# Performance work log

Measured on AMD Instinct MI355X. Metric: run time of the kernel, lower is better.

Reference implementation:

```python
import jax, jax.numpy as jnp
import numpy as np

B, S, H, L = 64, 512, 768, 21


def setup_inputs() -> dict:
    key = jax.random.key(0)
    ks = jax.random.split(key, 8)
    hidden = jax.random.normal(ks[0], (B, S, H), dtype=jnp.float32)
    attention_mask = jnp.ones((B, S), dtype=jnp.int32)
    labels = jax.random.randint(ks[1], (B, S), 0, L, dtype=jnp.int64)
    W = jax.random.normal(ks[2], (H, L), dtype=jnp.float32) * 0.02
    b = jnp.zeros((L,), dtype=jnp.float32)
    start_transitions = jax.random.uniform(ks[3], (L,), minval=-0.1, maxval=0.1)
    end_transitions = jax.random.uniform(ks[4], (L,), minval=-0.1, maxval=0.1)
    transitions = jax.random.uniform(ks[5], (L, L), minval=-0.1, maxval=0.1)
    return {"hidden": hidden, "attention_mask": attention_mask, "labels": labels,
            "W": W, "b": b, "start_transitions": start_transitions,
            "end_transitions": end_transitions, "transitions": transitions}


def _crf_llh(emissions, tags, mask, start, end, trans):
    # torchcrf log-likelihood, batch_first. emissions [B,S,L], tags [B,S], mask [B,S] bool
    maskf = mask.astype(emissions.dtype)
    first_tags = tags[:, 0]
    num = start[first_tags] + jnp.take_along_axis(emissions[:, 0], first_tags[:, None], axis=1)[:, 0]
    trans_scores = trans[tags[:, :-1], tags[:, 1:]]                         # [B,S-1]
    emit_scores = jnp.take_along_axis(emissions, tags[:, :, None], axis=2)[:, :, 0]  # [B,S]
    num = num + jnp.sum((trans_scores + emit_scores[:, 1:]) * maskf[:, 1:], axis=1)
    seq_ends = jnp.sum(mask.astype(jnp.int32), axis=1) - 1
    last_tags = jnp.take_along_axis(tags, seq_ends[:, None], axis=1)[:, 0]
    num = num + end[last_tags]
    # denominator: forward algorithm as a scan over time
    def step(score, xs):
        emit_t, m_t = xs  # [B,L], [B]
        nxt = jax.nn.logsumexp(score[:, :, None] + trans[None] + emit_t[:, None, :], axis=1)
        return jnp.where(m_t[:, None], nxt, score), None
    score0 = start[None] + emissions[:, 0]
    xs = (jnp.transpose(emissions[:, 1:], (1, 0, 2)), mask[:, 1:].T)
    scoreT, _ = jax.lax.scan(step, score0, xs)
    denom = jax.nn.logsumexp(scoreT + end[None], axis=1)
    return num - denom


def _viterbi_one_hot(emissions, mask, start, end, trans):
    # Viterbi decode (max-plus scan) + backtrack, returns one-hot logits like _decoded_to_one_hot
    def fstep(score, xs):
        emit_t, m_t = xs
        cand = score[:, :, None] + trans[None]     # [B,L,L]
        idx = jnp.argmax(cand, axis=1)             # [B,L] best previous tag
        nxt = jnp.max(cand, axis=1) + emit_t
        return jnp.where(m_t[:, None], nxt, score), idx
    score0 = start[None] + emissions[:, 0]
    xs = (jnp.transpose(emissions[:, 1:], (1, 0, 2)), mask[:, 1:].T)
    scoreT, hist = jax.lax.scan(fstep, score0, xs)   # hist [S-1,B,L]
    best_last = jnp.argmax(scoreT + end[None], axis=1)  # [B]
    def bstep(carry, xs):
        h_t, m_t = xs
        prev = jnp.take_along_axis(h_t, carry[:, None], axis=1)[:, 0]
        return jnp.where(m_t, prev, carry), carry
    tag0, tags_rest = jax.lax.scan(bstep, best_last, (hist, mask[:, 1:].T), reverse=True)
    tags = jnp.concatenate([tag0[:, None], tags_rest.T], axis=1)  # [B,S]
    one_hot = jax.nn.one_hot(tags, emissions.shape[-1], dtype=emissions.dtype)
    return one_hot * mask[:, :, None].astype(emissions.dtype)


def reference(hidden, attention_mask, labels, W, b, start_transitions, end_transitions, transitions):
    mask = attention_mask.astype(bool)
    emissions = jnp.einsum('bsh,hl->bsl', hidden, W) + b  # classifier (dropout = identity in eval)
    logits = _viterbi_one_hot(emissions, mask, start_transitions, end_transitions, transitions)
    # loss path: replicate forward's tag/mask fixups
    tags = jnp.where(labels < 0, 0, labels).at[:, 0].set(0)
    valid = (mask & (labels >= 0)).at[:, 0].set(True)
    llh = _crf_llh(emissions, tags, valid, start_transitions, end_transitions, transitions)
    loss = -jnp.mean(llh)
    return loss, logits
```

## Files before the change

kernel.cpp:

```cpp
#include <hip/hip_runtime.h>
#include <math.h>

#define BB 64
#define SS 512
#define HH 768
#define LL 21
#define STR 513
#define INFF __builtin_huge_valf()

__device__ inline float rlf(float v, int i) {
    return __int_as_float(__builtin_amdgcn_readlane(__float_as_int(v), i));
}
__device__ inline float mx3(float a, float b, float c) { return fmaxf(fmaxf(a, b), c); }
__device__ inline float wmax64(float v) {
    #pragma unroll
    for (int off = 32; off; off >>= 1) v = fmaxf(v, __shfl_xor(v, off));
    return v;
}
__device__ inline float rlmax21(float a) {
    float r0 = mx3(rlf(a, 0), rlf(a, 1), rlf(a, 2));
    float r1 = mx3(rlf(a, 3), rlf(a, 4), rlf(a, 5));
    float r2 = mx3(rlf(a, 6), rlf(a, 7), rlf(a, 8));
    float r3 = mx3(rlf(a, 9), rlf(a, 10), rlf(a, 11));
    float r4 = mx3(rlf(a, 12), rlf(a, 13), rlf(a, 14));
    float r5 = mx3(rlf(a, 15), rlf(a, 16), rlf(a, 17));
    float r6 = mx3(rlf(a, 18), rlf(a, 19), rlf(a, 20));
    return mx3(mx3(r0, r1, r2), mx3(r3, r4, r5), r6);
}

__global__ __launch_bounds__(128) void k_emis(const float* __restrict__ hidden,
                                              const float* __restrict__ W,
                                              const float* __restrict__ bias,
                                              float* __restrict__ em0,
                                              float* __restrict__ em1,
                                              float* __restrict__ em2,
                                              float* __restrict__ em3) {
    __shared__ float Wl[192 * 24];
    int tid = threadIdx.x;
    int q = blockIdx.x & 3;
    int rg = blockIdx.x >> 2;
    int row = rg * 128 + tid;
    const float* hp = hidden + (size_t)row * HH + q * 192;
    const float4* Wq4 = reinterpret_cast<const float4*>(W + q * 192 * LL);

    for (int f = tid; f < 1008; f += 128) {
        float4 v = Wq4[f];
        int e0 = 4 * f;
        { int e = e0,     k = e / 21, l = e - 21 * k; Wl[k * 24 + l] = v.x; }
        { int e = e0 + 1, k = e / 21, l = e - 21 * k; Wl[k * 24 + l] = v.y; }
        { int e = e0 + 2, k = e / 21, l = e - 21 * k; Wl[k * 24 + l] = v.z; }
        { int e = e0 + 3, k = e / 21, l = e - 21 * k; Wl[k * 24 + l] = v.w; }
    }
    __syncthreads();

    float acc[LL];
    #pragma unroll
    for (int l = 0; l < LL; ++l) acc[l] = 0.f;

#define FMAK(HV, WB) do { \
    float hv_ = (HV); \
    float4 q0 = *reinterpret_cast<const float4*>(WB); \
    float4 q1 = *reinterpret_cast<const float4*>((WB) + 4); \
    float4 q2 = *reinterpret_cast<const float4*>((WB) + 8); \
    float4 q3 = *reinterpret_cast<const float4*>((WB) + 12); \
    float4 q4 = *reinterpret_cast<const float4*>((WB) + 16); \
    float q20 = (WB)[20]; \
    acc[0]  = fmaf(hv_, q0.x, acc[0]);  acc[1]  = fmaf(hv_, q0.y, acc[1]); \
    acc[2]  = fmaf(hv_, q0.z, acc[2]);  acc[3]  = fmaf(hv_, q0.w, acc[3]); \
    acc[4]  = fmaf(hv_, q1.x, acc[4]);  acc[5]  = fmaf(hv_, q1.y, acc[5]); \
    acc[6]  = fmaf(hv_, q1.z, acc[6]);  acc[7]  = fmaf(hv_, q1.w, acc[7]); \
    acc[8]  = fmaf(hv_, q2.x, acc[8]);  acc[9]  = fmaf(hv_, q2.y, acc[9]); \
    acc[10] = fmaf(hv_, q2.z, acc[10]); acc[11] = fmaf(hv_, q2.w, acc[11]); \
    acc[12] = fmaf(hv_, q3.x, acc[12]); acc[13] = fmaf(hv_, q3.y, acc[13]); \
    acc[14] = fmaf(hv_, q3.z, acc[14]); acc[15] = fmaf(hv_, q3.w, acc[15]); \
    acc[16] = fmaf(hv_, q4.x, acc[16]); acc[17] = fmaf(hv_, q4.y, acc[17]); \
    acc[18] = fmaf(hv_, q4.z, acc[18]); acc[19] = fmaf(hv_, q4.w, acc[19]); \
    acc[20] = fmaf(hv_, q20, acc[20]); } while (0)

    float4 ha = *reinterpret_cast<const float4*>(hp);
    for (int c = 0; c < 48; ++c) {
        float4 hn = ha;
        if (c + 1 < 48) hn = *reinterpret_cast<const float4*>(hp + (c + 1) * 4);
        const float* wb = Wl + (c * 4) * 24;
        FMAK(ha.x, wb);
        FMAK(ha.y, wb + 24);
        FMAK(ha.z, wb + 48);
        FMAK(ha.w, wb + 72);
        ha = hn;
    }
#undef FMAK

    float* emr = (q == 0 ? em0 : q == 1 ? em1 : q == 2 ? em2 : em3) + (size_t)row * LL;
    if (q == 0) {
        #pragma unroll
        for (int l = 0; l < LL; ++l) emr[l] = acc[l] + bias[l];
    } else {
        #pragma unroll
        for (int l = 0; l < LL; ++l) emr[l] = acc[l];
    }
}

__global__ __launch_bounds__(64) void k_scan(const float* __restrict__ em0,
                                             const float* __restrict__ em1,
                                             const float* __restrict__ em2,
                                             const float* __restrict__ em3,
                                             const int* __restrict__ attn,
                                             const int* __restrict__ labels,
                                             const float* __restrict__ startT,
                                             const float* __restrict__ endT,
                                             const float* __restrict__ trans,
                                             float* __restrict__ num,
                                             float* __restrict__ denom,
                                             float* __restrict__ Sout) {
    __shared__ float eLT[LL * STR + 8];
    int lane = threadIdx.x;
    int bid = blockIdx.x;
    bool act = lane < LL;
    int jj = act ? lane : (LL - 1);

    if (bid < 128) {
        int b = bid & 63;
        size_t boff = (size_t)b * SS * LL;
        const float* emb0 = em0 + boff;
        const float* emb1 = em1 + boff;
        const float* emb2 = em2 + boff;
        const float* emb3 = em3 + boff;
        const int* mrow = attn + b * SS;

        for (int f = lane; f < (SS * LL) / 4; f += 64) {
            float4 v0 = *reinterpret_cast<const float4*>(emb0 + 4 * f);
            float4 v1 = *reinterpret_cast<const float4*>(emb1 + 4 * f);
            float4 v2 = *reinterpret_cast<const float4*>(emb2 + 4 * f);
            float4 v3 = *reinterpret_cast<const float4*>(emb3 + 4 * f);
            float4 v = make_float4((v0.x + v1.x) + (v2.x + v3.x),
                                   (v0.y + v1.y) + (v2.y + v3.y),
                                   (v0.z + v1.z) + (v2.z + v3.z),
                                   (v0.w + v1.w) + (v2.w + v3.w));
            unsigned e0 = 4u * (unsigned)f;
            { unsigned t = e0 / 21u,       j = e0 - 21u * t;       eLT[j * STR + t] = v.x; }
            { unsigned e = e0 + 1, t = e / 21u, j = e - 21u * t;   eLT[j * STR + t] = v.y; }
            { unsigned e = e0 + 2, t = e / 21u, j = e - 21u * t;   eLT[j * STR + t] = v.z; }
            { unsigned e = e0 + 3, t = e / 21u, j = e - 21u * t;   eLT[j * STR + t] = v.w; }
        }
        __syncthreads();

        int jbase = jj * STR;
        float A0, A1, A2, A3, B0, B1, B2, B3;

#define LDG(P, G) do { int t4_ = (G) * 4; \
    P##0 = eLT[jbase + t4_];     P##1 = eLT[jbase + t4_ + 1]; \
    P##2 = eLT[jbase + t4_ + 2]; P##3 = eLT[jbase + t4_ + 3]; } while (0)

        if (bid < 64) {
            float Tc[LL];
            #pragma unroll
            for (int i = 0; i < LL; ++i) Tc[i] = trans[i * LL + jj];
            float* Sgj = Sout + (size_t)b * (LL * SS) + jj * SS;

#define VCORE(EMIT, BIT) do { \
    float sv_[LL]; \
    _Pragma("unroll") for (int i_ = 0; i_ < LL; ++i_) sv_[i_] = rlf(a, i_); \
    __builtin_amdgcn_sched_barrier(0); \
    float cd_[LL]; \
    _Pragma("unroll") for (int i_ = 0; i_ < LL; ++i_) cd_[i_] = sv_[i_] + Tc[i_]; \
    float x0 = mx3(cd_[0], cd_[1], cd_[2]),   x1 = mx3(cd_[3], cd_[4], cd_[5]); \
    float x2 = mx3(cd_[6], cd_[7], cd_[8]),   x3 = mx3(cd_[9], cd_[10], cd_[11]); \
    float x4 = mx3(cd_[12], cd_[13], cd_[14]), x5 = mx3(cd_[15], cd_[16], cd_[17]); \
    float x6 = mx3(cd_[18], cd_[19], cd_[20]); \
    float best = mx3(mx3(x0, x1, x2), mx3(x3, x4, x5), x6); \
    bool mt_ = ((mm >> (BIT)) & 1ull) != 0ull; \
    float an_ = best + (EMIT); \
    a = (mt_ && act) ? an_ : a; \
} while (0)
#define VGROUPR(P, TB, BB0) do { \
    float o0_, o1_, o2_, o3_; \
    VCORE(P##0, (BB0));     o0_ = a; \
    VCORE(P##1, (BB0) + 1); o1_ = a; \
    VCORE(P##2, (BB0) + 2); o2_ = a; \
    VCORE(P##3, (BB0) + 3); o3_ = a; \
    if (act) *reinterpret_cast<float4*>(Sgj + (TB)) = make_float4(o0_, o1_, o2_, o3_); \
} while (0)

            LDG(A, 0); LDG(B, 1);
            int mk0 = mrow[lane];
            unsigned long long mm = __ballot(mk0 != 0);
            mk0 = mrow[64 + lane];
            float a = act ? (startT[lane] + A0) : -INFF;
            {
                float o0_ = a, o1_, o2_, o3_;
                VCORE(A1, 1); o1_ = a;
                VCORE(A2, 2); o2_ = a;
                VCORE(A3, 3); o3_ = a;
                if (act) *reinterpret_cast<float4*>(Sgj) = make_float4(o0_, o1_, o2_, o3_);
                LDG(A, 2);
                VGROUPR(B, 4, 4);
                LDG(B, 3);
            }
            for (int gg = 1; gg < 64; ++gg) {
                if ((gg & 7) == 0) {
                    mm = __ballot(mk0 != 0);
                    if (gg != 56) mk0 = mrow[((gg >> 3) + 1) * 64 + lane];
                }
                int bb = (gg & 7) * 8;
                VGROUPR(A, 8 * gg, bb);
                LDG(A, 2 * gg + 2);
                VGROUPR(B, 8 * gg + 4, bb + 4);
                LDG(B, 2 * gg + 3);
            }
#undef VCORE
#undef VGROUPR
        } else {
            float Ec[LL];
            #pragma unroll
            for (int i = 0; i < LL; ++i) Ec[i] = __expf(trans[i * LL + jj]);

#define LCORE(EMIT, BIT) do { \
    float x_ = __expf(a - M); \
    float sv_[LL]; \
    _Pragma("unroll") for (int i_ = 0; i_ < LL; ++i_) sv_[i_] = rlf(x_, i_); \
    __builtin_amdgcn_sched_barrier(0); \
    float g0_ = sv_[0] * Ec[0]; \
    _Pragma("unroll") for (int i_ = 1; i_ < 7; ++i_)  g0_ = fmaf(sv_[i_], Ec[i_], g0_); \
    float g1_ = sv_[7] * Ec[7]; \
    _Pragma("unroll") for (int i_ = 8; i_ < 14; ++i_) g1_ = fmaf(sv_[i_], Ec[i_], g1_); \
    float g2_ = sv_[14] * Ec[14]; \
    _Pragma("unroll") for (int i_ = 15; i_ < 21; ++i_) g2_ = fmaf(sv_[i_], Ec[i_], g2_); \
    float Ss_ = (g0_ + g1_) + g2_; \
    bool mt_ = ((mm >> (BIT)) & 1ull) != 0ull; \
    float an_ = M + __logf(Ss_) + (EMIT); \
    a = (mt_ && act) ? an_ : a; \
} while (0)

            LDG(A, 0); LDG(B, 1);
            int mk0 = mrow[lane];
            unsigned long long mm = __ballot(mk0 != 0);
            mk0 = mrow[64 + lane];
            float a = act ? (startT[lane] + A0) : -INFF;
            float M = rlmax21(a);
            {
                LCORE(A1, 1); LCORE(A2, 2); LCORE(A3, 3);
                LDG(A, 2);
                LCORE(B0, 4); LCORE(B1, 5); LCORE(B2, 6); LCORE(B3, 7);
                LDG(B, 3);
            }
            for (int gg = 1; gg < 64; ++gg) {
                if ((gg & 7) == 0) {
                    mm = __ballot(mk0 != 0);
                    if (gg != 56) mk0 = mrow[((gg >> 3) + 1) * 64 + lane];
                }
                M = rlmax21(a);
                int bb = (gg & 7) * 8;
                LCORE(A0, bb);     LCORE(A1, bb + 1); LCORE(A2, bb + 2); LCORE(A3, bb + 3);
                LDG(A, 2 * gg + 2);
                LCORE(B0, bb + 4); LCORE(B1, bb + 5); LCORE(B2, bb + 6); LCORE(B3, bb + 7);
                LDG(B, 2 * gg + 3);
            }
#undef LCORE
            float f = act ? (a + endT[lane]) : -INFF;
            float m = wmax64(f);
            float p = act ? __expf(f - m) : 0.f;
            #pragma unroll
            for (int off = 32; off; off >>= 1) p += __shfl_xor(p, off);
            if (lane == 0) denom[b] = m + __logf(p);
        }
#undef LDG
    } else {
        int b = bid - 128;
        const int* lrow = labels + b * SS;
        const int* arow = attn + b * SS;
        float psum = 0.f;
        int pcnt = 0;
        for (int s = 0; s < 8; ++s) {
            int t = s * 64 + lane;
            int lab = lrow[t];
            int mk = arow[t];
            int valid = (t == 0) ? 1 : ((mk != 0 && lab >= 0) ? 1 : 0);
            if (t >= 1 && valid) {
                int tag = (lab < 0) ? 0 : lab;
                int labp = lrow[t - 1];
                int tagp = (t == 1) ? 0 : ((labp < 0) ? 0 : labp);
                size_t ei = ((size_t)b * SS + t) * LL + tag;
                psum += trans[tagp * LL + tag] + ((em0[ei] + em1[ei]) + (em2[ei] + em3[ei]));
            }
            pcnt += valid;
        }
        #pragma unroll
        for (int off = 32; off; off >>= 1) {
            psum += __shfl_xor(psum, off);
            pcnt += __shfl_xor(pcnt, off);
        }
        int ts = pcnt - 1;
        int labL = lrow[ts];
        int tagL = (ts == 0) ? 0 : ((labL < 0) ? 0 : labL);
        if (lane == 0) {
            size_t e0i = (size_t)b * SS * LL;
            num[b] = startT[0] + ((em0[e0i] + em1[e0i]) + (em2[e0i] + em3[e0i]))
                   + psum + endT[tagL];
        }
    }
}

__global__ __launch_bounds__(512) void k_back(const float* __restrict__ S,
                                              const int* __restrict__ attn,
                                              const float* __restrict__ endT,
                                              const float* __restrict__ trans,
                                              int* __restrict__ tagsOut) {
    __shared__ float Sl[LL][517];
    __shared__ unsigned char pred[SS * 24];
    __shared__ unsigned char mapL[64 * 32];
    __shared__ float Tl[441];
    int tid = threadIdx.x, b = blockIdx.x;
    const float* SB = S + (size_t)b * (LL * SS);
    for (int i = tid; i < 441; i += 512) Tl[i] = trans[i];
    for (int f = tid; f < (LL * SS) / 4; f += 512) {
        float4 v = *reinterpret_cast<const float4*>(SB + 4 * f);
        int j = f >> 7, t0 = (f & 127) * 4;
        Sl[j][t0] = v.x; Sl[j][t0 + 1] = v.y; Sl[j][t0 + 2] = v.z; Sl[j][t0 + 3] = v.w;
    }
    __syncthreads();

    for (int u = tid; u < 511 * LL; u += 512) {
        int t = 1 + u / LL;
        int j = u - (u / LL) * LL;
        unsigned int pj = (unsigned int)j;
        if (attn[b * SS + t] != 0) {
            float bv = Sl[0][t - 1] + Tl[j];
            unsigned int bi = 0;
            #pragma unroll
            for (int i = 1; i < LL; ++i) {
                float c = Sl[i][t - 1] + Tl[i * LL + j];
                bool g = c > bv;
                bv = g ? c : bv;
                bi = g ? (unsigned int)i : bi;
            }
            pj = bi;
        }
        pred[t * 24 + j] = (unsigned char)pj;
    }
    __syncthreads();

    if (tid < 64) {
        int lane = tid;
        float f = (lane < LL) ? (Sl[lane][SS - 1] + endT[lane]) : -INFF;
        float m = wmax64(f);
        unsigned long long msk = __ballot(f == m);
        int best_last = __ffsll(msk) - 1;

        int tlo = 8 * lane + 1;
        int thi = 8 * lane + 8; if (thi > 511) thi = 511;
        unsigned int BM[LL];
        #pragma unroll
        for (int s = 0; s < LL; ++s) BM[s] = s;
        for (int k = 0; k < 8; ++k) {
            int t = thi - k;
            if (t >= tlo) {
                #pragma unroll
                for (int s = 0; s < LL; ++s) BM[s] = pred[t * 24 + BM[s]];
            }
        }
        #pragma unroll
        for (int s = 0; s < LL; ++s) mapL[lane * 32 + s] = (unsigned char)BM[s];

        #pragma unroll
        for (int kk = 1; kk < 64; kk <<= 1) {
            int p = lane + kk;
            bool vld = p < 64;
            int pp = vld ? p : 0;
            unsigned int P[LL];
            #pragma unroll
            for (int s = 0; s < LL; ++s) {
                unsigned int v = mapL[pp * 32 + s];
                P[s] = vld ? v : (unsigned int)s;
            }
            unsigned int N[LL];
            #pragma unroll
            for (int s = 0; s < LL; ++s) N[s] = mapL[lane * 32 + P[s]];
            #pragma unroll
            for (int s = 0; s < LL; ++s) mapL[lane * 32 + s] = (unsigned char)N[s];
        }

        int st8 = mapL[lane * 32 + best_last];
        int nxt = __shfl(st8, lane + 1);
        int cur = (lane == 63) ? best_last : nxt;
        for (int k = 0; k < 8; ++k) {
            int t = thi - k;
            if (t >= tlo) {
                tagsOut[b * SS + t] = cur;
                cur = pred[t * 24 + cur];
            }
        }
        if (lane == 0) tagsOut[b * SS] = cur;
    }
}

__global__ __launch_bounds__(256) void k_out(const float* __restrict__ num,
                                             const float* __restrict__ denom,
                                             const int* __restrict__ tagsW,
                                             const int* __restrict__ attn,
                                             float* __restrict__ out) {
    int gid = blockIdx.x * 256 + threadIdx.x;
    if ((int)blockIdx.x == (int)gridDim.x - 1 && threadIdx.x < 64) {
        float llh = num[threadIdx.x] - denom[threadIdx.x];
        #pragma unroll
        for (int off = 32; off; off >>= 1) llh += __shfl_xor(llh, off);
        if (threadIdx.x == 0) out[0] = -llh / (float)BB;
    }
    if (gid < BB * SS * LL) {
        int bt = gid / LL, l = gid % LL;
        int tag = tagsW[bt];
        int mk  = attn[bt];
        out[1 + gid] = (mk && tag == l) ? 1.f : 0.f;
    }
}

extern "C" void kernel_launch(void* const* d_in, const int* in_sizes, int n_in,
                              void* d_out, int out_size, void* d_ws, size_t ws_size,
                              hipStream_t stream) {
    const float* hidden = (const float*)d_in[0];
    const int*   attn   = (const int*)d_in[1];
    const int*   labels = (const int*)d_in[2];
    const float* W      = (const float*)d_in[3];
    const float* bias   = (const float*)d_in[4];
    const float* startT = (const float*)d_in[5];
    const float* endT   = (const float*)d_in[6];
    const float* trans  = (const float*)d_in[7];
    float* out = (float*)d_out;

    float* wsf   = (float*)d_ws;
    size_t emsz  = (size_t)BB * SS * LL;
    float* em0   = wsf;
    float* em1   = em0 + emsz;
    float* em2   = em1 + emsz;
    float* em3   = em2 + emsz;
    float* num   = em3 + emsz;
    float* denom = num + 64;
    int*   tags  = (int*)(denom + 64);
    float* Sbuf  = out + 4;

    hipLaunchKernelGGL(k_emis, dim3(1024), dim3(128), 0, stream, hidden, W, bias,
                       em0, em1, em2, em3);
    hipLaunchKernelGGL(k_scan, dim3(192), dim3(64),  0, stream, em0, em1, em2, em3,
                       attn, labels, startT, endT, trans, num, denom, Sbuf);
    hipLaunchKernelGGL(k_back, dim3(64),  dim3(512), 0, stream, Sbuf, attn, endT, trans, tags);
    int oh_blocks = (BB * SS * LL + 255) / 256;
    hipLaunchKernelGGL(k_out,  dim3(oh_blocks + 1), dim3(256), 0, stream,
                       num, denom, tags, attn, out);
}
```

Before: 149.0 us.

## Run Viterbi and forward scans in one wave halves; store emissions time-major

The Viterbi max-plus scan and the logsumexp forward scan for each batch now run in the two 32-lane halves of a single wavefront, so one block per batch covers both recurrences and the shared-memory emission load is done once instead of twice. The emission partials are written in a label-major [B][L][S] layout so the scan kernel can stage them with plain float4 copies instead of per-element divide-by-21 index math. The cost is divergent branches inside the wave: the two halves execute serially in the same instruction stream, which may lengthen the per-step critical path. The emission kernel's stores also become strided across labels.

```diff
diff --git a/kernel.cpp b/kernel.cpp
--- a/kernel.cpp
+++ b/kernel.cpp
@@ -17,14 +17,14 @@
     for (int off = 32; off; off >>= 1) v = fmaxf(v, __shfl_xor(v, off));
     return v;
 }
-__device__ inline float rlmax21(float a) {
-    float r0 = mx3(rlf(a, 0), rlf(a, 1), rlf(a, 2));
-    float r1 = mx3(rlf(a, 3), rlf(a, 4), rlf(a, 5));
-    float r2 = mx3(rlf(a, 6), rlf(a, 7), rlf(a, 8));
-    float r3 = mx3(rlf(a, 9), rlf(a, 10), rlf(a, 11));
-    float r4 = mx3(rlf(a, 12), rlf(a, 13), rlf(a, 14));
-    float r5 = mx3(rlf(a, 15), rlf(a, 16), rlf(a, 17));
-    float r6 = mx3(rlf(a, 18), rlf(a, 19), rlf(a, 20));
+__device__ inline float rlmax21h(float a) {
+    float r0 = mx3(rlf(a, 32), rlf(a, 33), rlf(a, 34));
+    float r1 = mx3(rlf(a, 35), rlf(a, 36), rlf(a, 37));
+    float r2 = mx3(rlf(a, 38), rlf(a, 39), rlf(a, 40));
+    float r3 = mx3(rlf(a, 41), rlf(a, 42), rlf(a, 43));
+    float r4 = mx3(rlf(a, 44), rlf(a, 45), rlf(a, 46));
+    float r5 = mx3(rlf(a, 47), rlf(a, 48), rlf(a, 49));
+    float r6 = mx3(rlf(a, 50), rlf(a, 51), rlf(a, 52));
     return mx3(mx3(r0, r1, r2), mx3(r3, r4, r5), r6);
 }
 
@@ -90,13 +90,16 @@
     }
 #undef FMAK
 
-    float* emr = (q == 0 ? em0 : q == 1 ? em1 : q == 2 ? em2 : em3) + (size_t)row * LL;
+    int bat = row >> 9;
+    int tpos = row & 511;
+    float* emq = (q == 0 ? em0 : q == 1 ? em1 : q == 2 ? em2 : em3)
+               + (size_t)bat * (LL * SS) + tpos;
     if (q == 0) {
         #pragma unroll
-        for (int l = 0; l < LL; ++l) emr[l] = acc[l] + bias[l];
+        for (int l = 0; l < LL; ++l) emq[l * SS] = acc[l] + bias[l];
     } else {
         #pragma unroll
-        for (int l = 0; l < LL; ++l) emr[l] = acc[l];
+        for (int l = 0; l < LL; ++l) emq[l * SS] = acc[l];
     }
 }
 
@@ -115,32 +118,29 @@
     __shared__ float eLT[LL * STR + 8];
     int lane = threadIdx.x;
     int bid = blockIdx.x;
-    bool act = lane < LL;
-    int jj = act ? lane : (LL - 1);
-
-    if (bid < 128) {
-        int b = bid & 63;
+    int lj = lane & 31;
+    bool actg = lj < LL;
+    int jj = actg ? lj : (LL - 1);
+    bool isV = lane < 32;
+
+    if (bid < 64) {
+        int b = bid;
         size_t boff = (size_t)b * SS * LL;
-        const float* emb0 = em0 + boff;
-        const float* emb1 = em1 + boff;
-        const float* emb2 = em2 + boff;
-        const float* emb3 = em3 + boff;
         const int* mrow = attn + b * SS;
 
         for (int f = lane; f < (SS * LL) / 4; f += 64) {
-            float4 v0 = *reinterpret_cast<const float4*>(emb0 + 4 * f);
-            float4 v1 = *reinterpret_cast<const float4*>(emb1 + 4 * f);
-            float4 v2 = *reinterpret_cast<const float4*>(emb2 + 4 * f);
-            float4 v3 = *reinterpret_cast<const float4*>(emb3 + 4 * f);
-            float4 v = make_float4((v0.x + v1.x) + (v2.x + v3.x),
-                                   (v0.y + v1.y) + (v2.y + v3.y),
-                                   (v0.z + v1.z) + (v2.z + v3.z),
-                                   (v0.w + v1.w) + (v2.w + v3.w));
-            unsigned e0 = 4u * (unsigned)f;
-            { unsigned t = e0 / 21u,       j = e0 - 21u * t;       eLT[j * STR + t] = v.x; }
-            { unsigned e = e0 + 1, t = e / 21u, j = e - 21u * t;   eLT[j * STR + t] = v.y; }
-            { unsigned e = e0 + 2, t = e / 21u, j = e - 21u * t;   eLT[j * STR + t] = v.z; }
-            { unsigned e = e0 + 3, t = e / 21u, j = e - 21u * t;   eLT[j * STR + t] = v.w; }
+            int j = f >> 7;
+            int t4 = (f & 127) * 4;
+            size_t go = boff + (size_t)j * SS + t4;
+            float4 v0 = *reinterpret_cast<const float4*>(em0 + go);
+            float4 v1 = *reinterpret_cast<const float4*>(em1 + go);
+            float4 v2 = *reinterpret_cast<const float4*>(em2 + go);
+            float4 v3 = *reinterpret_cast<const float4*>(em3 + go);
+            int base = j * STR + t4;
+            eLT[base]     = (v0.x + v1.x) + (v2.x + v3.x);
+            eLT[base + 1] = (v0.y + v1.y) + (v2.y + v3.y);
+            eLT[base + 2] = (v0.z + v1.z) + (v2.z + v3.z);
+            eLT[base + 3] = (v0.w + v1.w) + (v2.w + v3.w);
         }
         __syncthreads();
 
@@ -151,18 +151,20 @@
     P##0 = eLT[jbase + t4_];     P##1 = eLT[jbase + t4_ + 1]; \
     P##2 = eLT[jbase + t4_ + 2]; P##3 = eLT[jbase + t4_ + 3]; } while (0)
 
-        if (bid < 64) {
-            float Tc[LL];
-            #pragma unroll
-            for (int i = 0; i < LL; ++i) Tc[i] = trans[i * LL + jj];
-            float* Sgj = Sout + (size_t)b * (LL * SS) + jj * SS;
+        float Cc[LL];
+        #pragma unroll
+        for (int i = 0; i < LL; ++i) {
+            float tv = trans[i * LL + jj];
+            Cc[i] = isV ? tv : __expf(tv);
+        }
+        float* Sgj = Sout + (size_t)b * (LL * SS) + jj * SS;
 
 #define VCORE(EMIT, BIT) do { \
     float sv_[LL]; \
     _Pragma("unroll") for (int i_ = 0; i_ < LL; ++i_) sv_[i_] = rlf(a, i_); \
     __builtin_amdgcn_sched_barrier(0); \
     float cd_[LL]; \
-    _Pragma("unroll") for (int i_ = 0; i_ < LL; ++i_) cd_[i_] = sv_[i_] + Tc[i_]; \
+    _Pragma("unroll") for (int i_ = 0; i_ < LL; ++i_) cd_[i_] = sv_[i_] + Cc[i_]; \
     float x0 = mx3(cd_[0], cd_[1], cd_[2]),   x1 = mx3(cd_[3], cd_[4], cd_[5]); \
     float x2 = mx3(cd_[6], cd_[7], cd_[8]),   x3 = mx3(cd_[9], cd_[10], cd_[11]); \
     float x4 = mx3(cd_[12], cd_[13], cd_[14]), x5 = mx3(cd_[15], cd_[16], cd_[17]); \
@@ -170,7 +172,7 @@
     float best = mx3(mx3(x0, x1, x2), mx3(x3, x4, x5), x6); \
     bool mt_ = ((mm >> (BIT)) & 1ull) != 0ull; \
     float an_ = best + (EMIT); \
-    a = (mt_ && act) ? an_ : a; \
+    a = (mt_ && actg) ? an_ : a; \
 } while (0)
 #define VGROUPR(P, TB, BB0) do { \
     float o0_, o1_, o2_, o3_; \
@@ -178,94 +180,88 @@
     VCORE(P##1, (BB0) + 1); o1_ = a; \
     VCORE(P##2, (BB0) + 2); o2_ = a; \
     VCORE(P##3, (BB0) + 3); o3_ = a; \
-    if (act) *reinterpret_cast<float4*>(Sgj + (TB)) = make_float4(o0_, o1_, o2_, o3_); \
+    if (actg) *reinterpret_cast<float4*>(Sgj + (TB)) = make_float4(o0_, o1_, o2_, o3_); \
 } while (0)
-
-            LDG(A, 0); LDG(B, 1);
-            int mk0 = mrow[lane];
-            unsigned long long mm = __ballot(mk0 != 0);
-            mk0 = mrow[64 + lane];
-            float a = act ? (startT[lane] + A0) : -INFF;
-            {
-                float o0_ = a, o1_, o2_, o3_;
-                VCORE(A1, 1); o1_ = a;
-                VCORE(A2, 2); o2_ = a;
-                VCORE(A3, 3); o3_ = a;
-                if (act) *reinterpret_cast<float4*>(Sgj) = make_float4(o0_, o1_, o2_, o3_);
-                LDG(A, 2);
-                VGROUPR(B, 4, 4);
-                LDG(B, 3);
-            }
-            for (int gg = 1; gg < 64; ++gg) {
-                if ((gg & 7) == 0) {
-                    mm = __ballot(mk0 != 0);
-                    if (gg != 56) mk0 = mrow[((gg >> 3) + 1) * 64 + lane];
-                }
-                int bb = (gg & 7) * 8;
-                VGROUPR(A, 8 * gg, bb);
-                LDG(A, 2 * gg + 2);
-                VGROUPR(B, 8 * gg + 4, bb + 4);
-                LDG(B, 2 * gg + 3);
-            }
-#undef VCORE
-#undef VGROUPR
-        } else {
-            float Ec[LL];
-            #pragma unroll
-            for (int i = 0; i < LL; ++i) Ec[i] = __expf(trans[i * LL + jj]);
-
 #define LCORE(EMIT, BIT) do { \
     float x_ = __expf(a - M); \
     float sv_[LL]; \
-    _Pragma("unroll") for (int i_ = 0; i_ < LL; ++i_) sv_[i_] = rlf(x_, i_); \
+    _Pragma("unroll") for (int i_ = 0; i_ < LL; ++i_) sv_[i_] = rlf(x_, 32 + i_); \
     __builtin_amdgcn_sched_barrier(0); \
-    float g0_ = sv_[0] * Ec[0]; \
-    _Pragma("unroll") for (int i_ = 1; i_ < 7; ++i_)  g0_ = fmaf(sv_[i_], Ec[i_], g0_); \
-    float g1_ = sv_[7] * Ec[7]; \
-    _Pragma("unroll") for (int i_ = 8; i_ < 14; ++i_) g1_ = fmaf(sv_[i_], Ec[i_], g1_); \
-    float g2_ = sv_[14] * Ec[14]; \
-    _Pragma("unroll") for (int i_ = 15; i_ < 21; ++i_) g2_ = fmaf(sv_[i_], Ec[i_], g2_); \
+    float g0_ = sv_[0] * Cc[0]; \
+    _Pragma("unroll") for (int i_ = 1; i_ < 7; ++i_)  g0_ = fmaf(sv_[i_], Cc[i_], g0_); \
+    float g1_ = sv_[7] * Cc[7]; \
+    _Pragma("unroll") for (int i_ = 8; i_ < 14; ++i_) g1_ = fmaf(sv_[i_], Cc[i_], g1_); \
+    float g2_ = sv_[14] * Cc[14]; \
+    _Pragma("unroll") for (int i_ = 15; i_ < 21; ++i_) g2_ = fmaf(sv_[i_], Cc[i_], g2_); \
     float Ss_ = (g0_ + g1_) + g2_; \
     bool mt_ = ((mm >> (BIT)) & 1ull) != 0ull; \
     float an_ = M + __logf(Ss_) + (EMIT); \
-    a = (mt_ && act) ? an_ : a; \
+    a = (mt_ && actg) ? an_ : a; \
 } while (0)
 
-            LDG(A, 0); LDG(B, 1);
-            int mk0 = mrow[lane];
-            unsigned long long mm = __ballot(mk0 != 0);
-            mk0 = mrow[64 + lane];
-            float a = act ? (startT[lane] + A0) : -INFF;
-            float M = rlmax21(a);
-            {
-                LCORE(A1, 1); LCORE(A2, 2); LCORE(A3, 3);
-                LDG(A, 2);
-                LCORE(B0, 4); LCORE(B1, 5); LCORE(B2, 6); LCORE(B3, 7);
-                LDG(B, 3);
-            }
-            for (int gg = 1; gg < 64; ++gg) {
-                if ((gg & 7) == 0) {
-                    mm = __ballot(mk0 != 0);
-                    if (gg != 56) mk0 = mrow[((gg >> 3) + 1) * 64 + lane];
-                }
-                M = rlmax21(a);
-                int bb = (gg & 7) * 8;
-                LCORE(A0, bb);     LCORE(A1, bb + 1); LCORE(A2, bb + 2); LCORE(A3, bb + 3);
-                LDG(A, 2 * gg + 2);
+        LDG(A, 0); LDG(B, 1);
+        int mk0 = mrow[lane];
+        unsigned long long mm = __ballot(mk0 != 0);
+        mk0 = mrow[64 + lane];
+        float a = actg ? (startT[jj] + A0) : -INFF;
+        float M = 0.f;
+
+        if (isV) {
+            float o0_ = a, o1_, o2_, o3_;
+            VCORE(A1, 1); o1_ = a;
+            VCORE(A2, 2); o2_ = a;
+            VCORE(A3, 3); o3_ = a;
+            if (actg) *reinterpret_cast<float4*>(Sgj) = make_float4(o0_, o1_, o2_, o3_);
+        } else {
+            M = rlmax21h(a);
+            LCORE(A1, 1); LCORE(A2, 2); LCORE(A3, 3);
+        }
+        LDG(A, 2);
+        if (isV) {
+            VGROUPR(B, 4, 4);
+        } else {
+            LCORE(B0, 4); LCORE(B1, 5); LCORE(B2, 6); LCORE(B3, 7);
+        }
+        LDG(B, 3);
+
+        for (int gg = 1; gg < 64; ++gg) {
+            if ((gg & 7) == 0) {
+                mm = __ballot(mk0 != 0);
+                if (gg != 56) mk0 = mrow[((gg >> 3) + 1) * 64 + lane];
+            }
+            int bb = (gg & 7) * 8;
+            if (isV) {
+                VGROUPR(A, 8 * gg, bb);
+            } else {
+                M = rlmax21h(a);
+                LCORE(A0, bb); LCORE(A1, bb + 1); LCORE(A2, bb + 2); LCORE(A3, bb + 3);
+            }
+            LDG(A, 2 * gg + 2);
+            if (isV) {
+                VGROUPR(B, 8 * gg + 4, bb + 4);
+            } else {
                 LCORE(B0, bb + 4); LCORE(B1, bb + 5); LCORE(B2, bb + 6); LCORE(B3, bb + 7);
-                LDG(B, 2 * gg + 3);
-            }
+            }
+            LDG(B, 2 * gg + 3);
+        }
+#undef VCORE
+#undef VGROUPR
 #undef LCORE
-            float f = act ? (a + endT[lane]) : -INFF;
-            float m = wmax64(f);
-            float p = act ? __expf(f - m) : 0.f;
-            #pragma unroll
-            for (int off = 32; off; off >>= 1) p += __shfl_xor(p, off);
-            if (lane == 0) denom[b] = m + __logf(p);
-        }
 #undef LDG
+
+        if (!isV) {
+            float f = actg ? (a + endT[jj]) : -INFF;
+            float m = f;
+            #pragma unroll
+            for (int off = 16; off; off >>= 1) m = fmaxf(m, __shfl_xor(m, off));
+            float p = actg ? __expf(f - m) : 0.f;
+            #pragma unroll
+            for (int off = 16; off; off >>= 1) p += __shfl_xor(p, off);
+            if (lane == 32) denom[b] = m + __logf(p);
+        }
     } else {
-        int b = bid - 128;
+        int b = bid - 64;
+        size_t boff = (size_t)b * SS * LL;
         const int* lrow = labels + b * SS;
         const int* arow = attn + b * SS;
         float psum = 0.f;
@@ -279,7 +275,7 @@
                 int tag = (lab < 0) ? 0 : lab;
                 int labp = lrow[t - 1];
                 int tagp = (t == 1) ? 0 : ((labp < 0) ? 0 : labp);
-                size_t ei = ((size_t)b * SS + t) * LL + tag;
+                size_t ei = boff + (size_t)tag * SS + t;
                 psum += trans[tagp * LL + tag] + ((em0[ei] + em1[ei]) + (em2[ei] + em3[ei]));
             }
             pcnt += valid;
@@ -293,8 +289,7 @@
         int labL = lrow[ts];
         int tagL = (ts == 0) ? 0 : ((labL < 0) ? 0 : labL);
         if (lane == 0) {
-            size_t e0i = (size_t)b * SS * LL;
-            num[b] = startT[0] + ((em0[e0i] + em1[e0i]) + (em2[e0i] + em3[e0i]))
+            num[b] = startT[0] + ((em0[boff] + em1[boff]) + (em2[boff] + em3[boff]))
                    + psum + endT[tagL];
         }
     }
@@ -439,7 +434,7 @@
 
     hipLaunchKernelGGL(k_emis, dim3(1024), dim3(128), 0, stream, hidden, W, bias,
                        em0, em1, em2, em3);
-    hipLaunchKernelGGL(k_scan, dim3(192), dim3(64),  0, stream, em0, em1, em2, em3,
+    hipLaunchKernelGGL(k_scan, dim3(128), dim3(64),  0, stream, em0, em1, em2, em3,
                        attn, labels, startT, endT, trans, num, denom, Sbuf);
     hipLaunchKernelGGL(k_back, dim3(64),  dim3(512), 0, stream, Sbuf, attn, endT, trans, tags);
     int oh_blocks = (BB * SS * LL + 255) / 256;
```

Result: slower. 252.9 us (+69.7%).
